# Optimization experiments

Measured on AMD Instinct MI355X. Metric: run time of the kernel, lower is better.

Reference implementation:

```python
import jax, jax.numpy as jnp
import numpy as np

HO, WO = 64, 64
SHARPNESS = 150.0


def _stereographic_grid(ho, wo):
    # Matches create_normal_grid(..., 'stereographic'); torch.meshgrid 'ij':
    # v varies over rows (ho), u over cols (wo).
    v, u = np.meshgrid(np.arange(ho), np.arange(wo), indexing='ij')
    p = 4.0 * ((u + 0.5) / wo - 0.5)
    q = -4.0 * ((v + 0.5) / ho - 0.5)
    d = 1.0 + p ** 2 + q ** 2
    z = -(-1.0 + p ** 2 + q ** 2) / d
    m = (z > 0.0).astype(np.float32)
    x = 2.0 * p / d * m
    y = 2.0 * q / d * m
    z = z * m
    return np.stack([x, y, z], axis=-1).reshape(-1, 3).astype(np.float32)  # [ho*wo,3]


_GRID = _stereographic_grid(HO, WO)
_IDX = np.nonzero(np.any(_GRID != 0, axis=-1))[0]  # static valid-query indices [N]
_QN = _GRID[_IDX]  # [N,3]


def setup_inputs() -> dict:
    key = jax.random.key(0)
    k1, k2, k3 = jax.random.split(key, 3)
    bs, c, h, w = 2, 64, 192, 192
    in_fea_map = jax.random.normal(k1, (bs, c, h, w), dtype=jnp.float32)
    nrm = jax.random.normal(k2, (bs, 3, h, w), dtype=jnp.float32)
    in_normal_map = nrm / (jnp.linalg.norm(nrm, axis=1, keepdims=True) + 1e-8)
    in_mask_map = (jax.random.uniform(k3, (bs, 1, h, w)) > 0.2).astype(jnp.float32)
    log_query_norm = jnp.full((1,), np.log(SHARPNESS), dtype=jnp.float32)
    return {"in_fea_map": in_fea_map, "in_normal_map": in_normal_map,
            "in_mask_map": in_mask_map, "log_query_norm": log_query_norm}


def reference(in_fea_map, in_normal_map, in_mask_map, log_query_norm):
    bs, c, h, w = in_fea_map.shape
    hw = h * w
    qn = jnp.asarray(_QN, dtype=in_fea_map.dtype)  # [N,3] static valid queries
    vals = in_fea_map.reshape(bs, c, hw).transpose(0, 2, 1)       # [bs,HW,c]
    key_n = in_normal_map.reshape(bs, 3, hw)                       # [bs,3,HW]
    cos = jnp.einsum('nd,bdm->bnm', qn, key_n)                     # [bs,N,HW]
    dps = cos / np.float32(np.sqrt(3.0))
    dps = dps - jnp.max(dps, axis=-1, keepdims=True)
    w_ = jnp.exp(jnp.exp(log_query_norm) * dps)                    # dropout in eval = identity
    w_ = w_ * in_mask_map.reshape(bs, 1, hw)
    weights = w_ / (jnp.sum(w_, axis=-1, keepdims=True) + 1e-9)    # [bs,N,HW]
    mapped = weights @ vals                                        # [bs,N,c]
    mapped = jnp.concatenate([jnp.broadcast_to(qn, (bs,) + qn.shape), mapped], axis=-1)
    # variance map over last 3 feature channels
    mean = mapped[..., -3:]
    sq_mean = weights @ (vals[..., -3:] ** 2)
    var = jnp.sum(sq_mean - mean ** 2, axis=-1, keepdims=True)
    mapped = jnp.concatenate([var, mapped], axis=-1)
    # cosine map
    rm_cos = jnp.sum(weights * cos, axis=-1, keepdims=True)
    mapped = jnp.concatenate([rm_cos, mapped], axis=-1)            # [bs,N,c+5]
    C = mapped.shape[-1]
    out = jnp.zeros((bs, HO * WO, C), mapped.dtype).at[:, _IDX, :].set(mapped)
    return out.transpose(0, 2, 1).reshape(bs, C, HO, WO)
```

## Files before the change

kernel.cpp:

```cpp
#include <hip/hip_runtime.h>
#include <hip/hip_bf16.h>
#include <cstdint>
#include <cstddef>

#define HW 36864
#define QT 64
#define NCHA 69
#define NCHK 576

constexpr bool is_valid_px(int v, int u) {
  int a = 2 * u - 63, b = 2 * v - 63;
  return a * a + b * b < 1024;
}
constexpr int count_valid() {
  int n = 0;
  for (int v = 0; v < 64; ++v)
    for (int u = 0; u < 64; ++u)
      if (is_valid_px(v, u)) ++n;
  return n;
}
constexpr int NV  = count_valid();
constexpr int NQT = (NV + QT - 1) / QT;
constexpr int NQP = NQT * QT;
constexpr int PLANE = 2 * NQP * NCHA;

constexpr size_t BM_SHORTS  = (size_t)2 * NCHK * 80 * 64;
constexpr size_t BM_BYTES   = BM_SHORTS * 2;
constexpr size_t NV_BYTES   = (size_t)2 * HW * 4 * 4;
constexpr size_t PART_OFF   = BM_BYTES + NV_BYTES;

struct QTab {
  short idx[NQP];
  short rank[4096];
};
constexpr QTab make_qtab() {
  QTab t{};
  int n = 0;
  for (int p = 0; p < 4096; ++p) {
    int v = p >> 6, u = p & 63;
    if (is_valid_px(v, u)) { t.idx[n] = (short)p; t.rank[p] = (short)n; ++n; }
    else t.rank[p] = -1;
  }
  for (int i = n; i < NQP; ++i) t.idx[i] = -1;
  return t;
}
__constant__ QTab g_qtab = make_qtab();

typedef short short8 __attribute__((ext_vector_type(8)));
typedef float f32x4  __attribute__((ext_vector_type(4)));

__device__ __forceinline__ unsigned short f2b(float f) {
  unsigned int u = __float_as_uint(f);
  u += 0x7FFFu + ((u >> 16) & 1u);
  return (unsigned short)(u >> 16);
}
__device__ __forceinline__ ushort2 f2b2(float a, float b) {
  __hip_bfloat162 h = __float22bfloat162_rn(make_float2(a, b));
  return *(ushort2*)&h;
}
__device__ __forceinline__ void pix2qn(int pix, float& x, float& y, float& z) {
  x = 0.f; y = 0.f; z = 0.f;
  if (pix >= 0) {
    int v = pix >> 6, u = pix & 63;
    float p = (float)(2 * u - 63) * (1.0f / 32.0f);
    float q = -(float)(2 * v - 63) * (1.0f / 32.0f);
    float d = 1.0f + p * p + q * q;
    x = 2.0f * p / d; y = 2.0f * q / d; z = (1.0f - p * p - q * q) / d;
  }
}

#define PREP_BM_BLKS 2880
#define PREP_NV_BLKS 288

__global__ __launch_bounds__(256) void prep_kernel(
    const float* __restrict__ fea,
    const float* __restrict__ nrm,
    const float* __restrict__ msk,
    const float* __restrict__ lqn,
    unsigned short* __restrict__ Bm,
    float* __restrict__ nv)
{
  const float Cc = __expf(lqn[0]) * 0.57735026919f;
  if (blockIdx.x < PREP_BM_BLKS) {
    int gid = blockIdx.x * 256 + threadIdx.x;
    int g   = gid & 7;
    int row = (gid >> 3) % 80;
    int chk = ((gid >> 3) / 80) % NCHK;
    int b   = gid / (8 * 80 * NCHK);
    int px0 = chk * 64 + g * 8;
    float v[8];
    if (row < 64) {
      const float* p = fea + ((size_t)b * 64 + row) * HW + px0;
      #pragma unroll
      for (int i = 0; i < 8; ++i) v[i] = p[i];
    } else if (row < 67) {
      const float* p = fea + ((size_t)b * 64 + (61 + row - 64)) * HW + px0;
      #pragma unroll
      for (int i = 0; i < 8; ++i) { float x = p[i]; v[i] = x * x; }
    } else if (row < 70) {
      const float* p = nrm + ((size_t)b * 3 + (row - 67)) * HW + px0;
      #pragma unroll
      for (int i = 0; i < 8; ++i) v[i] = p[i];
    } else {
      float c = (row == 70) ? 1.0f : 0.0f;
      #pragma unroll
      for (int i = 0; i < 8; ++i) v[i] = c;
    }
    short8 o;
    #pragma unroll
    for (int p2 = 0; p2 < 4; ++p2) {
      ushort2 pr = f2b2(v[2 * p2], v[2 * p2 + 1]);
      o[2 * p2] = (short)pr.x; o[2 * p2 + 1] = (short)pr.y;
    }
    *(short8*)&Bm[(((size_t)b * NCHK + chk) * 80 + row) * 64 + g * 8] = o;
  } else {
    int p = (blockIdx.x - PREP_BM_BLKS) * 256 + threadIdx.x;
    int b = p / HW, px = p % HW;
    float nx = nrm[((size_t)b * 3 + 0) * HW + px];
    float ny = nrm[((size_t)b * 3 + 1) * HW + px];
    float nz = nrm[((size_t)b * 3 + 2) * HW + px];
    float mk = msk[(size_t)b * HW + px];
    float bias = -Cc + (mk > 0.5f ? 0.f : -2000.f);
    *(float4*)&nv[(size_t)p * 4] = make_float4(Cc * nx, Cc * ny, Cc * nz, bias);
  }
}

template<int KSC>
__global__ __launch_bounds__(256, 4) void partial_kernel(
    const unsigned short* __restrict__ Bm,
    const float* __restrict__ nv,
    float* __restrict__ part)
{
  constexpr int SLICE  = HW / KSC;
  constexpr int NCHUNK = SLICE / 64;

  __shared__ __align__(16) unsigned short v_s[2][80][72];
  __shared__ __align__(16) float nrm4_s[2][64][4];

  const int bx  = blockIdx.x;
  const int cls = bx & 7;
  const int r0  = bx >> 3;
  const int qt  = r0 % NQT;
  const int sh  = r0 / NQT;
  const int s   = sh * 8 + cls;
  const int b   = s / KSC;
  const int ks  = s % KSC;

  const int t    = threadIdx.x;
  const int wv   = t >> 6;
  const int Mh   = wv & 1;
  const int kko  = (wv >> 1) * 32;
  const int l    = t & 63;
  const int lq   = l >> 4;
  const int mrow = l & 15;

  float qx[2], qy[2], qz[2];
  pix2qn(g_qtab.idx[qt * QT + 32 * Mh + mrow],      qx[0], qy[0], qz[0]);
  pix2qn(g_qtab.idx[qt * QT + 32 * Mh + 16 + mrow], qx[1], qy[1], qz[1]);

  const int g0r = t >> 3,          g0c = (t & 7) * 8;
  const int g1r = (t + 256) >> 3,  g1c = g0c;
  const int g2r = (t + 512) >> 3;
  const int pxp = 32 * (l >> 5) + 4 * (l & 7) + ((l >> 3) & 3);

  f32x4 acc[2][5];
  #pragma unroll
  for (int h = 0; h < 2; ++h)
    #pragma unroll
    for (int nt = 0; nt < 5; ++nt) acc[h][nt] = (f32x4)(0.0f);

  short8 pB[3];
  float4 pnv;

  auto load_chunk = [&](int ck) {
    int chkAbs = ks * NCHUNK + ck;
    const unsigned short* src = Bm + ((size_t)b * NCHK + chkAbs) * (80 * 64);
    pB[0] = *(const short8*)(src + (size_t)(t)       * 8);
    pB[1] = *(const short8*)(src + (size_t)(t + 256) * 8);
    if (t < 128) pB[2] = *(const short8*)(src + (size_t)(t + 512) * 8);
    if (t < 64)  pnv = *(const float4*)&nv[((size_t)b * HW + chkAbs * 64 + l) * 4];
  };
  auto store_chunk = [&](int buf) {
    *(short8*)&v_s[buf][g0r][g0c] = pB[0];
    *(short8*)&v_s[buf][g1r][g1c] = pB[1];
    if (t < 128) *(short8*)&v_s[buf][g2r][g0c] = pB[2];
    if (t < 64)  *(float4*)&nrm4_s[buf][pxp][0] = pnv;
  };

  load_chunk(0);
  store_chunk(0);
  __syncthreads();

  for (int ck = 0; ck < NCHUNK; ++ck) {
    const int buf = ck & 1;
    if (ck + 1 < NCHUNK) load_chunk(ck + 1);

    float e0[8], e1[8];
    #pragma unroll
    for (int j = 0; j < 8; ++j) {
      const float4 nvv = *(const float4*)&nrm4_s[buf][kko + 4 * j + lq][0];
      float t0 = fmaf(qx[0], nvv.x, fmaf(qy[0], nvv.y, fmaf(qz[0], nvv.z, nvv.w)));
      float t1 = fmaf(qx[1], nvv.x, fmaf(qy[1], nvv.y, fmaf(qz[1], nvv.z, nvv.w)));
      e0[j] = __expf(t0);
      e1[j] = __expf(t1);
    }
    short8 a0, a1;
    #pragma unroll
    for (int p = 0; p < 4; ++p) {
      ushort2 p0 = f2b2(e0[2 * p], e0[2 * p + 1]);
      ushort2 p1 = f2b2(e1[2 * p], e1[2 * p + 1]);
      a0[2 * p] = (short)p0.x; a0[2 * p + 1] = (short)p0.y;
      a1[2 * p] = (short)p1.x; a1[2 * p + 1] = (short)p1.y;
    }
    #pragma unroll
    for (int nt = 0; nt < 5; ++nt) {
      short8 bb = *(const short8*)&v_s[buf][16 * nt + mrow][kko + 8 * lq];
      acc[0][nt] = __builtin_amdgcn_mfma_f32_16x16x32_bf16(a0, bb, acc[0][nt], 0, 0, 0);
      acc[1][nt] = __builtin_amdgcn_mfma_f32_16x16x32_bf16(a1, bb, acc[1][nt], 0, 0, 0);
    }

    if (ck + 1 < NCHUNK) {
      store_chunk(buf ^ 1);
      __syncthreads();
    }
  }

  __syncthreads();
  float* scr = (float*)&v_s[0][0][0];
  float* exs = scr + 64 * 80;

  if (kko) {
    #pragma unroll
    for (int h = 0; h < 2; ++h)
      #pragma unroll
      for (int nt = 0; nt < 5; ++nt)
        #pragma unroll
        for (int rr = 0; rr < 4; ++rr) {
          int qloc = 32 * Mh + 16 * h + 4 * lq + rr;
          scr[qloc * 80 + 16 * nt + mrow] = acc[h][nt][rr];
        }
  }
  __syncthreads();
  const size_t pbase = (size_t)ks * PLANE + ((size_t)b * NQP + (size_t)(qt * QT)) * NCHA;
  if (!kko) {
    #pragma unroll
    for (int h = 0; h < 2; ++h) {
      #pragma unroll
      for (int nt = 0; nt < 5; ++nt)
        #pragma unroll
        for (int rr = 0; rr < 4; ++rr) {
          int qloc = 32 * Mh + 16 * h + 4 * lq + rr;
          acc[h][nt][rr] += scr[qloc * 80 + 16 * nt + mrow];
        }
      #pragma unroll
      for (int nt = 0; nt < 4; ++nt)
        #pragma unroll
        for (int rr = 0; rr < 4; ++rr) {
          int qloc = 32 * Mh + 16 * h + 4 * lq + rr;
          part[pbase + (size_t)qloc * NCHA + (size_t)(16 * nt + mrow)] = acc[h][nt][rr];
        }
      if (mrow < 7) {
        #pragma unroll
        for (int rr = 0; rr < 4; ++rr)
          exs[(32 * Mh + 16 * h + 4 * lq + rr) * 9 + mrow] = acc[h][4][rr];
      }
    }
  }
  __syncthreads();
  if (t < 64) {
    float gx, gy, gz;
    pix2qn(g_qtab.idx[qt * QT + t], gx, gy, gz);
    const float* E = exs + t * 9;
    float swc = gx * E[3] + gy * E[4] + gz * E[5];
    size_t o = pbase + (size_t)t * NCHA;
    part[o + 64] = E[0];
    part[o + 65] = E[1];
    part[o + 66] = E[2];
    part[o + 67] = swc;
    part[o + 68] = E[6];
  }
}

#define NFIN (2 * NQT * 8)
#define NTAIL (2 * NFIN)

__global__ __launch_bounds__(256) void finalize_kernel(
    const float* __restrict__ part,
    float* __restrict__ out,
    int ksc)
{
  const int blk = blockIdx.x;
  const int t   = threadIdx.x;

  if (blk < NFIN) {
    __shared__ float sm[8][NCHA];
    const int b   = blk / (NQT * 8);
    const int rem = blk % (NQT * 8);
    const int qt  = rem >> 3;
    const int qr  = rem & 7;
    const int q0  = qt * QT + qr * 8;

    const size_t colbase = ((size_t)b * NQP + (size_t)q0) * NCHA;
    for (int i = t; i < 8 * NCHA; i += 256) {
      float sv = 0.f;
      const size_t off = colbase + (size_t)i;
      #pragma unroll 8
      for (int k = 0; k < ksc; ++k) sv += part[(size_t)k * PLANE + off];
      sm[0][i] = sv;
    }
    __syncthreads();

    for (int i = t; i < 8 * NCHA; i += 256) {
      const int ql = i / NCHA;
      const int oc = i % NCHA;
      const int pix = g_qtab.idx[q0 + ql];
      if (pix < 0) continue;
      const float* A = sm[ql];
      const float inv = 1.0f / (A[68] + 1e-9f);
      float gx, gy, gz;
      pix2qn(pix, gx, gy, gz);
      float val;
      if (oc == 0)      val = A[67] * inv;
      else if (oc == 1) {
        val = 0.f;
        #pragma unroll
        for (int j = 0; j < 3; ++j) {
          float m  = A[61 + j] * inv;
          float sq = A[64 + j] * inv;
          val += sq - m * m;
        }
      }
      else if (oc == 2) val = gx;
      else if (oc == 3) val = gy;
      else if (oc == 4) val = gz;
      else              val = A[oc - 5] * inv;
      out[((size_t)b * NCHA + (size_t)oc) * 4096 + pix] = val;
    }
  } else {
    const int start = (blk - NFIN) * 256 + t;
    const int strd  = (NTAIL - NFIN) * 256;
    const int TOT   = 2 * NCHA * 4096;
    for (int i = start; i < TOT; i += strd) {
      if (g_qtab.rank[i & 4095] < 0) out[i] = 0.0f;
    }
  }
}

extern "C" void kernel_launch(void* const* d_in, const int* in_sizes, int n_in,
                              void* d_out, int out_size, void* d_ws, size_t ws_size,
                              hipStream_t stream) {
  const float* fea = (const float*)d_in[0];
  const float* nrm = (const float*)d_in[1];
  const float* msk = (const float*)d_in[2];
  const float* lqn = (const float*)d_in[3];
  unsigned short* Bm = (unsigned short*)d_ws;
  float* nv   = (float*)((char*)d_ws + BM_BYTES);
  float* part = (float*)((char*)d_ws + PART_OFF);
  float* out  = (float*)d_out;

  prep_kernel<<<dim3(PREP_BM_BLKS + PREP_NV_BLKS), 256, 0, stream>>>(
      fea, nrm, msk, lqn, Bm, nv);

  const size_t need64 = PART_OFF + (size_t)PLANE * 64 * sizeof(float);
  const size_t need32 = PART_OFF + (size_t)PLANE * 32 * sizeof(float);
  if (ws_size >= need64) {
    partial_kernel<64><<<dim3(2 * 64 * NQT), 256, 0, stream>>>(Bm, nv, part);
    finalize_kernel<<<dim3(NTAIL), 256, 0, stream>>>(part, out, 64);
  } else if (ws_size >= need32) {
    partial_kernel<32><<<dim3(2 * 32 * NQT), 256, 0, stream>>>(Bm, nv, part);
    finalize_kernel<<<dim3(NTAIL), 256, 0, stream>>>(part, out, 32);
  } else {
    partial_kernel<16><<<dim3(2 * 16 * NQT), 256, 0, stream>>>(Bm, nv, part);
    finalize_kernel<<<dim3(NTAIL), 256, 0, stream>>>(part, out, 16);
  }
}
```

Baseline: 117.3 us.

## Double query tile to 128 so each block reuses staged values across more queries

Raises the query tile from 64 to 128. Each wave now covers four 16-row query subtiles instead of two, so every staged key/value chunk in shared memory feeds twice as many MFMAs and global loads of Bm drop by half. The cross-wave reduction epilogue is restructured into two rounds of shared-scratch exchange, and finalize indexing is adjusted to match. Costs: more accumulator registers (occupancy hint lowered from 4 to 3 blocks), fewer blocks, more padded queries in the last tile, and a longer serialized epilogue.

```diff
diff --git a/kernel.cpp b/kernel.cpp
--- a/kernel.cpp
+++ b/kernel.cpp
@@ -4,7 +4,7 @@
 #include <cstddef>
 
 #define HW 36864
-#define QT 64
+#define QT 128
 #define NCHA 69
 #define NCHK 576
 
@@ -49,11 +49,6 @@
 typedef short short8 __attribute__((ext_vector_type(8)));
 typedef float f32x4  __attribute__((ext_vector_type(4)));
 
-__device__ __forceinline__ unsigned short f2b(float f) {
-  unsigned int u = __float_as_uint(f);
-  u += 0x7FFFu + ((u >> 16) & 1u);
-  return (unsigned short)(u >> 16);
-}
 __device__ __forceinline__ ushort2 f2b2(float a, float b) {
   __hip_bfloat162 h = __float22bfloat162_rn(make_float2(a, b));
   return *(ushort2*)&h;
@@ -126,7 +121,7 @@
 }
 
 template<int KSC>
-__global__ __launch_bounds__(256, 4) void partial_kernel(
+__global__ __launch_bounds__(256, 3) void partial_kernel(
     const unsigned short* __restrict__ Bm,
     const float* __restrict__ nv,
     float* __restrict__ part)
@@ -154,20 +149,21 @@
   const int lq   = l >> 4;
   const int mrow = l & 15;
 
-  float qx[2], qy[2], qz[2];
-  pix2qn(g_qtab.idx[qt * QT + 32 * Mh + mrow],      qx[0], qy[0], qz[0]);
-  pix2qn(g_qtab.idx[qt * QT + 32 * Mh + 16 + mrow], qx[1], qy[1], qz[1]);
+  float qx[4], qy[4], qz[4];
+  #pragma unroll
+  for (int st = 0; st < 4; ++st)
+    pix2qn(g_qtab.idx[qt * QT + 64 * Mh + 16 * st + mrow], qx[st], qy[st], qz[st]);
 
   const int g0r = t >> 3,          g0c = (t & 7) * 8;
-  const int g1r = (t + 256) >> 3,  g1c = g0c;
+  const int g1r = (t + 256) >> 3;
   const int g2r = (t + 512) >> 3;
   const int pxp = 32 * (l >> 5) + 4 * (l & 7) + ((l >> 3) & 3);
 
-  f32x4 acc[2][5];
+  f32x4 acc[4][5];
   #pragma unroll
-  for (int h = 0; h < 2; ++h)
-    #pragma unroll
-    for (int nt = 0; nt < 5; ++nt) acc[h][nt] = (f32x4)(0.0f);
+  for (int st = 0; st < 4; ++st)
+    #pragma unroll
+    for (int nt = 0; nt < 5; ++nt) acc[st][nt] = (f32x4)(0.0f);
 
   short8 pB[3];
   float4 pnv;
@@ -182,7 +178,7 @@
   };
   auto store_chunk = [&](int buf) {
     *(short8*)&v_s[buf][g0r][g0c] = pB[0];
-    *(short8*)&v_s[buf][g1r][g1c] = pB[1];
+    *(short8*)&v_s[buf][g1r][g0c] = pB[1];
     if (t < 128) *(short8*)&v_s[buf][g2r][g0c] = pB[2];
     if (t < 64)  *(float4*)&nrm4_s[buf][pxp][0] = pnv;
   };
@@ -195,28 +191,30 @@
     const int buf = ck & 1;
     if (ck + 1 < NCHUNK) load_chunk(ck + 1);
 
-    float e0[8], e1[8];
+    float ee[4][8];
     #pragma unroll
     for (int j = 0; j < 8; ++j) {
       const float4 nvv = *(const float4*)&nrm4_s[buf][kko + 4 * j + lq][0];
-      float t0 = fmaf(qx[0], nvv.x, fmaf(qy[0], nvv.y, fmaf(qz[0], nvv.z, nvv.w)));
-      float t1 = fmaf(qx[1], nvv.x, fmaf(qy[1], nvv.y, fmaf(qz[1], nvv.z, nvv.w)));
-      e0[j] = __expf(t0);
-      e1[j] = __expf(t1);
-    }
-    short8 a0, a1;
-    #pragma unroll
-    for (int p = 0; p < 4; ++p) {
-      ushort2 p0 = f2b2(e0[2 * p], e0[2 * p + 1]);
-      ushort2 p1 = f2b2(e1[2 * p], e1[2 * p + 1]);
-      a0[2 * p] = (short)p0.x; a0[2 * p + 1] = (short)p0.y;
-      a1[2 * p] = (short)p1.x; a1[2 * p + 1] = (short)p1.y;
-    }
+      #pragma unroll
+      for (int st = 0; st < 4; ++st) {
+        float tt = fmaf(qx[st], nvv.x, fmaf(qy[st], nvv.y, fmaf(qz[st], nvv.z, nvv.w)));
+        ee[st][j] = __expf(tt);
+      }
+    }
+    short8 a[4];
+    #pragma unroll
+    for (int st = 0; st < 4; ++st)
+      #pragma unroll
+      for (int p = 0; p < 4; ++p) {
+        ushort2 pr = f2b2(ee[st][2 * p], ee[st][2 * p + 1]);
+        a[st][2 * p] = (short)pr.x; a[st][2 * p + 1] = (short)pr.y;
+      }
     #pragma unroll
     for (int nt = 0; nt < 5; ++nt) {
       short8 bb = *(const short8*)&v_s[buf][16 * nt + mrow][kko + 8 * lq];
-      acc[0][nt] = __builtin_amdgcn_mfma_f32_16x16x32_bf16(a0, bb, acc[0][nt], 0, 0, 0);
-      acc[1][nt] = __builtin_amdgcn_mfma_f32_16x16x32_bf16(a1, bb, acc[1][nt], 0, 0, 0);
+      #pragma unroll
+      for (int st = 0; st < 4; ++st)
+        acc[st][nt] = __builtin_amdgcn_mfma_f32_16x16x32_bf16(a[st], bb, acc[st][nt], 0, 0, 0);
     }
 
     if (ck + 1 < NCHUNK) {
@@ -227,61 +225,101 @@
 
   __syncthreads();
   float* scr = (float*)&v_s[0][0][0];
-  float* exs = scr + 64 * 80;
-
-  if (kko) {
-    #pragma unroll
-    for (int h = 0; h < 2; ++h)
+  float* exs = (float*)&nrm4_s[0][0][0];
+
+  const size_t pbase = (size_t)ks * PLANE + ((size_t)b * NQP + (size_t)(qt * QT)) * NCHA;
+
+  if (wv == 2) {
+    #pragma unroll
+    for (int st = 0; st < 4; ++st)
       #pragma unroll
       for (int nt = 0; nt < 5; ++nt)
         #pragma unroll
-        for (int rr = 0; rr < 4; ++rr) {
-          int qloc = 32 * Mh + 16 * h + 4 * lq + rr;
-          scr[qloc * 80 + 16 * nt + mrow] = acc[h][nt][rr];
-        }
-  }
-  __syncthreads();
-  const size_t pbase = (size_t)ks * PLANE + ((size_t)b * NQP + (size_t)(qt * QT)) * NCHA;
-  if (!kko) {
-    #pragma unroll
-    for (int h = 0; h < 2; ++h) {
+        for (int rr = 0; rr < 4; ++rr)
+          scr[(16 * st + 4 * lq + rr) * 80 + 16 * nt + mrow] = acc[st][nt][rr];
+  }
+  __syncthreads();
+  if (wv == 0) {
+    #pragma unroll
+    for (int st = 0; st < 4; ++st) {
       #pragma unroll
       for (int nt = 0; nt < 5; ++nt)
         #pragma unroll
-        for (int rr = 0; rr < 4; ++rr) {
-          int qloc = 32 * Mh + 16 * h + 4 * lq + rr;
-          acc[h][nt][rr] += scr[qloc * 80 + 16 * nt + mrow];
-        }
+        for (int rr = 0; rr < 4; ++rr)
+          acc[st][nt][rr] += scr[(16 * st + 4 * lq + rr) * 80 + 16 * nt + mrow];
       #pragma unroll
       for (int nt = 0; nt < 4; ++nt)
         #pragma unroll
-        for (int rr = 0; rr < 4; ++rr) {
-          int qloc = 32 * Mh + 16 * h + 4 * lq + rr;
-          part[pbase + (size_t)qloc * NCHA + (size_t)(16 * nt + mrow)] = acc[h][nt][rr];
-        }
+        for (int rr = 0; rr < 4; ++rr)
+          part[pbase + (size_t)(16 * st + 4 * lq + rr) * NCHA + (size_t)(16 * nt + mrow)]
+              = acc[st][nt][rr];
       if (mrow < 7) {
         #pragma unroll
         for (int rr = 0; rr < 4; ++rr)
-          exs[(32 * Mh + 16 * h + 4 * lq + rr) * 9 + mrow] = acc[h][4][rr];
+          exs[(16 * st + 4 * lq + rr) * 7 + mrow] = acc[st][4][rr];
       }
     }
   }
   __syncthreads();
-  if (t < 64) {
+  if (wv == 1) {
     float gx, gy, gz;
-    pix2qn(g_qtab.idx[qt * QT + t], gx, gy, gz);
-    const float* E = exs + t * 9;
+    pix2qn(g_qtab.idx[qt * QT + l], gx, gy, gz);
+    const float* E = exs + l * 7;
     float swc = gx * E[3] + gy * E[4] + gz * E[5];
-    size_t o = pbase + (size_t)t * NCHA;
+    size_t o = pbase + (size_t)l * NCHA;
     part[o + 64] = E[0];
     part[o + 65] = E[1];
     part[o + 66] = E[2];
     part[o + 67] = swc;
     part[o + 68] = E[6];
   }
-}
-
-#define NFIN (2 * NQT * 8)
+  if (wv == 3) {
+    #pragma unroll
+    for (int st = 0; st < 4; ++st)
+      #pragma unroll
+      for (int nt = 0; nt < 5; ++nt)
+        #pragma unroll
+        for (int rr = 0; rr < 4; ++rr)
+          scr[(16 * st + 4 * lq + rr) * 80 + 16 * nt + mrow] = acc[st][nt][rr];
+  }
+  __syncthreads();
+  if (wv == 1) {
+    #pragma unroll
+    for (int st = 0; st < 4; ++st) {
+      #pragma unroll
+      for (int nt = 0; nt < 5; ++nt)
+        #pragma unroll
+        for (int rr = 0; rr < 4; ++rr)
+          acc[st][nt][rr] += scr[(16 * st + 4 * lq + rr) * 80 + 16 * nt + mrow];
+      #pragma unroll
+      for (int nt = 0; nt < 4; ++nt)
+        #pragma unroll
+        for (int rr = 0; rr < 4; ++rr)
+          part[pbase + (size_t)(64 + 16 * st + 4 * lq + rr) * NCHA + (size_t)(16 * nt + mrow)]
+              = acc[st][nt][rr];
+      if (mrow < 7) {
+        #pragma unroll
+        for (int rr = 0; rr < 4; ++rr)
+          exs[(16 * st + 4 * lq + rr) * 7 + mrow] = acc[st][4][rr];
+      }
+    }
+  }
+  __syncthreads();
+  if (wv == 0) {
+    float gx, gy, gz;
+    pix2qn(g_qtab.idx[qt * QT + 64 + l], gx, gy, gz);
+    const float* E = exs + l * 7;
+    float swc = gx * E[3] + gy * E[4] + gz * E[5];
+    size_t o = pbase + (size_t)(64 + l) * NCHA;
+    part[o + 64] = E[0];
+    part[o + 65] = E[1];
+    part[o + 66] = E[2];
+    part[o + 67] = swc;
+    part[o + 68] = E[6];
+  }
+}
+
+#define NFIN (2 * NQP / 8)
 #define NTAIL (2 * NFIN)
 
 __global__ __launch_bounds__(256) void finalize_kernel(
@@ -294,11 +332,9 @@
 
   if (blk < NFIN) {
     __shared__ float sm[8][NCHA];
-    const int b   = blk / (NQT * 8);
-    const int rem = blk % (NQT * 8);
-    const int qt  = rem >> 3;
-    const int qr  = rem & 7;
-    const int q0  = qt * QT + qr * 8;
+    const int b   = blk / (NQP / 8);
+    const int rem = blk % (NQP / 8);
+    const int q0  = rem * 8;
 
     const size_t colbase = ((size_t)b * NQP + (size_t)q0) * NCHA;
     for (int i = t; i < 8 * NCHA; i += 256) {
```

New measurement: 121.7 us. 3.7% more time.
